# Optimization experiments

Measured on AMD Instinct MI355X. Metric: run time of the kernel, lower is better.

The kernel has to match this reference:

```python
import jax, jax.numpy as jnp
import numpy as np

ALPHA = 0.2  # leaky relu negative slope


def setup_inputs() -> dict:
    key = jax.random.key(0)
    ks = jax.random.split(key, 6)
    B, K, F = 8, 256, 64
    E = 2 * F  # gatv2 embed dim
    x = jax.random.normal(ks[0], (B, K, F), dtype=jnp.float32)
    lin_w = jax.random.normal(ks[1], (E, 2 * F), dtype=jnp.float32) * 0.05
    lin_b = jax.random.normal(ks[2], (E,), dtype=jnp.float32) * 0.05
    a = jax.random.normal(ks[3], (E, 1), dtype=jnp.float32) * 0.05
    att_bias = jnp.zeros((K, K), dtype=jnp.float32)
    fc_w = jax.random.normal(ks[4], (64, F), dtype=jnp.float32) * 0.05
    fc_b = jax.random.normal(ks[5], (64,), dtype=jnp.float32) * 0.05
    return {"x": x, "lin_w": lin_w, "lin_b": lin_b, "a": a,
            "att_bias": att_bias, "fc_w": fc_w, "fc_b": fc_b}


def reference(x, lin_w, lin_b, a, att_bias, fc_w, fc_b):
    # GATv2 temporal attention. Original builds a_input[b,i,j] = concat(x[b,i], x[b,j])
    # then lin(a_input). Since lin is linear, decompose W = [W1 | W2] so that
    # lin(concat(xi, xj)) = xi @ W1^T + xj @ W2^T + b  -- identical math,
    # avoids the [B,K,K,2F] concat tensor.
    F_dim = x.shape[-1]
    w1 = lin_w[:, :F_dim]   # [E, F] applied to the repeated (i) block
    w2 = lin_w[:, F_dim:]   # [E, F] applied to the alternating (j) block
    s_i = jnp.einsum('bkf,ef->bke', x, w1)           # [B,K,E]
    s_j = jnp.einsum('bkf,ef->bke', x, w2)           # [B,K,E]
    hidden = s_i[:, :, None, :] + s_j[:, None, :, :] + lin_b  # [B,K,K,E]
    hidden = jnp.where(hidden >= 0, hidden, ALPHA * hidden)   # leaky relu
    e = jnp.einsum('bije,e->bij', hidden, a[:, 0])            # [B,K,K]
    e = e + att_bias                                           # bias [K,K]
    attention = jax.nn.softmax(e, axis=2)
    # dropout p=0.0 -> identity
    h = jax.nn.sigmoid(jnp.einsum('bij,bjf->bif', attention, x))  # [B,K,F]
    return jnp.einsum('bkf,of->bko', h, fc_w) + fc_b              # [B,K,out_dim]
```

## Files before the change

kernel.cpp:

```cpp
#include <hip/hip_runtime.h>
#include <hip/hip_bf16.h>

#define ALPHA 0.2f
constexpr int B = 8, K = 256, F = 64, E = 128;


__device__ __forceinline__ float term4(float4 aa, float4 uu, float4 vv, float acc) {
    acc = fmaf(aa.x, fabsf(uu.x + vv.x), acc);
    acc = fmaf(aa.y, fabsf(uu.y + vv.y), acc);
    acc = fmaf(aa.z, fabsf(uu.z + vv.z), acc);
    acc = fmaf(aa.w, fabsf(uu.w + vv.w), acc);
    return acc;
}

__global__ __launch_bounds__(256) void gat_kA(
    const float* __restrict__ x, const float* __restrict__ lin_w,
    const float* __restrict__ lin_b, const float* __restrict__ a,
    const float* __restrict__ fc_w,
    float* __restrict__ u, float* __restrict__ vT,
    float* __restrict__ c, float* __restrict__ d,
    float4* __restrict__ fcp)
{
    const int t = threadIdx.x;
    const int wave = t >> 6, lane = t & 63;
    const int row0 = blockIdx.x * 4;
    const int e = t & 127, rh = t >> 7;
    const int b = row0 >> 8;

    __shared__ float4 wls[4096];
    __shared__ alignas(16) float xs[4 * F];
    __shared__ float redA[4][4];

    const float4* lw4 = (const float4*)lin_w;
#pragma unroll
    for (int i = 0; i < 16; ++i) {
        int idx = i * 256 + t;
        int ee = idx >> 5, cc = idx & 31;
        wls[(ee << 5) | (cc ^ (ee & 31))] = lw4[idx];
    }
    xs[t] = x[row0 * F + t];

    if (blockIdx.x == 0) {
#pragma unroll
        for (int i = 0; i < 4; ++i) {
            int k = i * 256 + t;
            int f4 = k >> 6, o = k & 63;
            const float* r = fc_w + o * F + f4 * 4;
            fcp[k] = make_float4(r[0], r[1], r[2], r[3]);
        }
    }
    __syncthreads();

    const int ebase = e << 5, ex = e & 31;
    const float* xr0 = &xs[(rh * 2) * F];
    const float* xr1 = &xs[(rh * 2 + 1) * F];
    float a10 = 0.f, a11 = 0.f, a20 = 0.f, a21 = 0.f;
#pragma unroll
    for (int p = 0; p < 16; ++p) {
        float4 w1 = wls[ebase + (p ^ ex)];
        float4 w2 = wls[ebase + ((16 | p) ^ ex)];
        float4 xv0 = *(const float4*)&xr0[4 * p];
        float4 xv1 = *(const float4*)&xr1[4 * p];
        a10 = fmaf(w1.x, xv0.x, a10); a10 = fmaf(w1.y, xv0.y, a10);
        a10 = fmaf(w1.z, xv0.z, a10); a10 = fmaf(w1.w, xv0.w, a10);
        a20 = fmaf(w2.x, xv0.x, a20); a20 = fmaf(w2.y, xv0.y, a20);
        a20 = fmaf(w2.z, xv0.z, a20); a20 = fmaf(w2.w, xv0.w, a20);
        a11 = fmaf(w1.x, xv1.x, a11); a11 = fmaf(w1.y, xv1.y, a11);
        a11 = fmaf(w1.z, xv1.z, a11); a11 = fmaf(w1.w, xv1.w, a11);
        a21 = fmaf(w2.x, xv1.x, a21); a21 = fmaf(w2.y, xv1.y, a21);
        a21 = fmaf(w2.z, xv1.z, a21); a21 = fmaf(w2.w, xv1.w, a21);
    }
    const float bb = lin_b[e], av = a[e];
    const float u0 = a10 + bb, u1 = a11 + bb;
    const int r0 = row0 + rh * 2;
    u[r0 * E + e] = u0;
    u[(r0 + 1) * E + e] = u1;
    const int kk = r0 & (K - 1);
    float* vbase = vT + ((b * 32 + (e >> 2)) * K) * 4 + (e & 3);
    vbase[kk * 4] = a20;
    vbase[(kk + 1) * 4] = a21;

    float vals[4] = {av * a20, av * u0, av * a21, av * u1};
#pragma unroll
    for (int off = 32; off; off >>= 1) {
#pragma unroll
        for (int q = 0; q < 4; ++q) vals[q] += __shfl_xor(vals[q], off);
    }
    if (lane == 0) {
        redA[wave][0] = vals[0]; redA[wave][1] = vals[1];
        redA[wave][2] = vals[2]; redA[wave][3] = vals[3];
    }
    __syncthreads();
    if (t < 8) {
        int r = t >> 1, w = t & 1;
        int wp = (r >> 1) * 2, q = (r & 1) * 2 + w;
        float val = redA[wp][q] + redA[wp + 1][q];
        if (w == 0) c[row0 + r] = val; else d[row0 + r] = val;
    }
}

__global__ __launch_bounds__(256) void gat_kB(
    const float* __restrict__ x, const float* __restrict__ a,
    const float* __restrict__ att_bias, const float4* __restrict__ fcp,
    const float* __restrict__ fc_b, const float* __restrict__ u,
    const float4* __restrict__ vT4, const float* __restrict__ c,
    const float* __restrict__ d, float* __restrict__ out)
{
    const int blk = blockIdx.x;
    const int b = blk >> 6;
    const int i0 = (blk & 63) * 4;
    const int t = threadIdx.x;
    const int wave = t >> 6, lane = t & 63;

    __shared__ float part[4][4][K];
    __shared__ float ps[4][K];
    __shared__ float4 hpart[4][4][16];
    __shared__ float4 h4s[4][16];

    {
        const int eq = wave, jj = lane;
        const float4* v4  = vT4 + (size_t)b * 32 * K + (size_t)eq * 8 * K + jj;
        const float4* u4g = (const float4*)(u + (size_t)(b * K + i0) * E);
        const float4* a4g = (const float4*)a;
        float ej[4][4];
#pragma unroll
        for (int i = 0; i < 4; ++i)
#pragma unroll
            for (int q = 0; q < 4; ++q) ej[i][q] = 0.f;

#pragma unroll 2
        for (int it = 0; it < 8; ++it) {
            const int e4 = eq * 8 + it;
            float4 aa  = a4g[e4];
            float4 uu0 = u4g[0 * 32 + e4];
            float4 uu1 = u4g[1 * 32 + e4];
            float4 uu2 = u4g[2 * 32 + e4];
            float4 uu3 = u4g[3 * 32 + e4];
            float4 vv0 = v4[it * K + 0 * 64];
            float4 vv1 = v4[it * K + 1 * 64];
            float4 vv2 = v4[it * K + 2 * 64];
            float4 vv3 = v4[it * K + 3 * 64];
            ej[0][0] = term4(aa, uu0, vv0, ej[0][0]); ej[0][1] = term4(aa, uu0, vv1, ej[0][1]);
            ej[0][2] = term4(aa, uu0, vv2, ej[0][2]); ej[0][3] = term4(aa, uu0, vv3, ej[0][3]);
            ej[1][0] = term4(aa, uu1, vv0, ej[1][0]); ej[1][1] = term4(aa, uu1, vv1, ej[1][1]);
            ej[1][2] = term4(aa, uu1, vv2, ej[1][2]); ej[1][3] = term4(aa, uu1, vv3, ej[1][3]);
            ej[2][0] = term4(aa, uu2, vv0, ej[2][0]); ej[2][1] = term4(aa, uu2, vv1, ej[2][1]);
            ej[2][2] = term4(aa, uu2, vv2, ej[2][2]); ej[2][3] = term4(aa, uu2, vv3, ej[2][3]);
            ej[3][0] = term4(aa, uu3, vv0, ej[3][0]); ej[3][1] = term4(aa, uu3, vv1, ej[3][1]);
            ej[3][2] = term4(aa, uu3, vv2, ej[3][2]); ej[3][3] = term4(aa, uu3, vv3, ej[3][3]);
        }
#pragma unroll
        for (int i = 0; i < 4; ++i)
#pragma unroll
            for (int q = 0; q < 4; ++q)
                part[eq][i][q * 64 + jj] = ej[i][q];
    }
    __syncthreads();

    {
        const int w = wave;
        const float dw = d[b * K + i0 + w];
        float ex[4], ssum = 0.f;
#pragma unroll
        for (int q = 0; q < 4; ++q) {
            const int j = q * 64 + lane;
            float s = part[0][w][j] + part[1][w][j] + part[2][w][j] + part[3][w][j];
            float cv = c[b * K + j];
            float av = att_bias[(i0 + w) * K + j];
            float e  = fmaf(0.4f, s, fmaf(0.6f, dw + cv, av));
            ex[q] = __expf(e);
            ssum += ex[q];
        }
#pragma unroll
        for (int off = 32; off; off >>= 1) ssum += __shfl_xor(ssum, off);
        const float inv = 1.f / ssum;
#pragma unroll
        for (int q = 0; q < 4; ++q) ps[w][q * 64 + lane] = ex[q] * inv;
    }
    __syncthreads();

    {
        const int jg = t >> 4, fq = t & 15;
        const float4* xb4 = (const float4*)x + (size_t)b * K * 16 + fq;
        const float4* ps4 = (const float4*)ps;
        float4 h0 = make_float4(0,0,0,0), h1 = h0, h2 = h0, h3 = h0;
#pragma unroll
        for (int j4 = 0; j4 < 4; ++j4) {
            float4 p0 = ps4[0 * 64 + jg * 4 + j4];
            float4 p1 = ps4[1 * 64 + jg * 4 + j4];
            float4 p2 = ps4[2 * 64 + jg * 4 + j4];
            float4 p3 = ps4[3 * 64 + jg * 4 + j4];
            const int j = jg * 16 + j4 * 4;
            float4 xa = xb4[(size_t)(j + 0) * 16];
            float4 xb = xb4[(size_t)(j + 1) * 16];
            float4 xc = xb4[(size_t)(j + 2) * 16];
            float4 xd = xb4[(size_t)(j + 3) * 16];
            h0.x = fmaf(p0.x, xa.x, h0.x); h0.y = fmaf(p0.x, xa.y, h0.y); h0.z = fmaf(p0.x, xa.z, h0.z); h0.w = fmaf(p0.x, xa.w, h0.w);
            h0.x = fmaf(p0.y, xb.x, h0.x); h0.y = fmaf(p0.y, xb.y, h0.y); h0.z = fmaf(p0.y, xb.z, h0.z); h0.w = fmaf(p0.y, xb.w, h0.w);
            h0.x = fmaf(p0.z, xc.x, h0.x); h0.y = fmaf(p0.z, xc.y, h0.y); h0.z = fmaf(p0.z, xc.z, h0.z); h0.w = fmaf(p0.z, xc.w, h0.w);
            h0.x = fmaf(p0.w, xd.x, h0.x); h0.y = fmaf(p0.w, xd.y, h0.y); h0.z = fmaf(p0.w, xd.z, h0.z); h0.w = fmaf(p0.w, xd.w, h0.w);
            h1.x = fmaf(p1.x, xa.x, h1.x); h1.y = fmaf(p1.x, xa.y, h1.y); h1.z = fmaf(p1.x, xa.z, h1.z); h1.w = fmaf(p1.x, xa.w, h1.w);
            h1.x = fmaf(p1.y, xb.x, h1.x); h1.y = fmaf(p1.y, xb.y, h1.y); h1.z = fmaf(p1.y, xb.z, h1.z); h1.w = fmaf(p1.y, xb.w, h1.w);
            h1.x = fmaf(p1.z, xc.x, h1.x); h1.y = fmaf(p1.z, xc.y, h1.y); h1.z = fmaf(p1.z, xc.z, h1.z); h1.w = fmaf(p1.z, xc.w, h1.w);
            h1.x = fmaf(p1.w, xd.x, h1.x); h1.y = fmaf(p1.w, xd.y, h1.y); h1.z = fmaf(p1.w, xd.z, h1.z); h1.w = fmaf(p1.w, xd.w, h1.w);
            h2.x = fmaf(p2.x, xa.x, h2.x); h2.y = fmaf(p2.x, xa.y, h2.y); h2.z = fmaf(p2.x, xa.z, h2.z); h2.w = fmaf(p2.x, xa.w, h2.w);
            h2.x = fmaf(p2.y, xb.x, h2.x); h2.y = fmaf(p2.y, xb.y, h2.y); h2.z = fmaf(p2.y, xb.z, h2.z); h2.w = fmaf(p2.y, xb.w, h2.w);
            h2.x = fmaf(p2.z, xc.x, h2.x); h2.y = fmaf(p2.z, xc.y, h2.y); h2.z = fmaf(p2.z, xc.z, h2.z); h2.w = fmaf(p2.z, xc.w, h2.w);
            h2.x = fmaf(p2.w, xd.x, h2.x); h2.y = fmaf(p2.w, xd.y, h2.y); h2.z = fmaf(p2.w, xd.z, h2.z); h2.w = fmaf(p2.w, xd.w, h2.w);
            h3.x = fmaf(p3.x, xa.x, h3.x); h3.y = fmaf(p3.x, xa.y, h3.y); h3.z = fmaf(p3.x, xa.z, h3.z); h3.w = fmaf(p3.x, xa.w, h3.w);
            h3.x = fmaf(p3.y, xb.x, h3.x); h3.y = fmaf(p3.y, xb.y, h3.y); h3.z = fmaf(p3.y, xb.z, h3.z); h3.w = fmaf(p3.y, xb.w, h3.w);
            h3.x = fmaf(p3.z, xc.x, h3.x); h3.y = fmaf(p3.z, xc.y, h3.y); h3.z = fmaf(p3.z, xc.z, h3.z); h3.w = fmaf(p3.z, xc.w, h3.w);
            h3.x = fmaf(p3.w, xd.x, h3.x); h3.y = fmaf(p3.w, xd.y, h3.y); h3.z = fmaf(p3.w, xd.z, h3.z); h3.w = fmaf(p3.w, xd.w, h3.w);
        }
#pragma unroll
        for (int off = 16; off <= 32; off <<= 1) {
            h0.x += __shfl_xor(h0.x, off); h0.y += __shfl_xor(h0.y, off);
            h0.z += __shfl_xor(h0.z, off); h0.w += __shfl_xor(h0.w, off);
            h1.x += __shfl_xor(h1.x, off); h1.y += __shfl_xor(h1.y, off);
            h1.z += __shfl_xor(h1.z, off); h1.w += __shfl_xor(h1.w, off);
            h2.x += __shfl_xor(h2.x, off); h2.y += __shfl_xor(h2.y, off);
            h2.z += __shfl_xor(h2.z, off); h2.w += __shfl_xor(h2.w, off);
            h3.x += __shfl_xor(h3.x, off); h3.y += __shfl_xor(h3.y, off);
            h3.z += __shfl_xor(h3.z, off); h3.w += __shfl_xor(h3.w, off);
        }
        if (lane < 16) {
            hpart[wave][0][lane] = h0; hpart[wave][1][lane] = h1;
            hpart[wave][2][lane] = h2; hpart[wave][3][lane] = h3;
        }
    }
    __syncthreads();
    if (t < 64) {
        const int i = t >> 4, f4 = t & 15;
        float4 A = hpart[0][i][f4], Bq = hpart[1][i][f4];
        float4 C = hpart[2][i][f4], D = hpart[3][i][f4];
        float4 hv;
        hv.x = A.x + Bq.x + C.x + D.x; hv.y = A.y + Bq.y + C.y + D.y;
        hv.z = A.z + Bq.z + C.z + D.z; hv.w = A.w + Bq.w + C.w + D.w;
        hv.x = 1.f / (1.f + __expf(-hv.x)); hv.y = 1.f / (1.f + __expf(-hv.y));
        hv.z = 1.f / (1.f + __expf(-hv.z)); hv.w = 1.f / (1.f + __expf(-hv.w));
        h4s[i][f4] = hv;
    }
    __syncthreads();

    {
        float acc = 0.f;
#pragma unroll
        for (int f4 = 0; f4 < 16; ++f4) {
            float4 hv = h4s[wave][f4];
            float4 wv = fcp[f4 * 64 + lane];
            acc = fmaf(hv.x, wv.x, acc); acc = fmaf(hv.y, wv.y, acc);
            acc = fmaf(hv.z, wv.z, acc); acc = fmaf(hv.w, wv.w, acc);
        }
        out[(b * K + i0 + wave) * F + lane] = acc + fc_b[lane];
    }
}

extern "C" void kernel_launch(void* const* d_in, const int* in_sizes, int n_in,
                              void* d_out, int out_size, void* d_ws, size_t ws_size,
                              hipStream_t stream) {
    const float* x        = (const float*)d_in[0];
    const float* lin_w    = (const float*)d_in[1];
    const float* lin_b    = (const float*)d_in[2];
    const float* a        = (const float*)d_in[3];
    const float* att_bias = (const float*)d_in[4];
    const float* fc_w     = (const float*)d_in[5];
    const float* fc_b     = (const float*)d_in[6];
    float* out = (float*)d_out;

    float* u   = (float*)d_ws;
    float* vT  = u + B * K * E;
    float* c   = vT + B * K * E;
    float* d   = c + B * K;
    float4* fcp = (float4*)(d + B * K);

    gat_kA<<<B * K / 4, 256, 0, stream>>>(x, lin_w, lin_b, a, fc_w,
                                          u, vT, c, d, fcp);
    gat_kB<<<B * K / 4, 256, 0, stream>>>(x, a, att_bias, fcp, fc_b, u,
                                          (const float4*)vT, c, d, out);
}
```

Baseline: 23.85 us.

## Process eight rows per block in both kernels to raise weight and v reuse

Kernel A now computes eight rows per block instead of four, so each block's 64KB LDS load of lin_w serves twice as many rows and the grid is halved. Kernel B moves to 512-thread blocks that each handle eight query rows, with each wave covering a quarter of the previous embedding slice. This lets each v load be reused across eight u rows and halves redundant loads of v and x across blocks. In exchange there are fewer blocks (256), higher register pressure from the 8x4 accumulators, and larger shared memory use (part alone is 64KB), which may limit occupancy.

```diff
diff --git a/kernel.cpp b/kernel.cpp
--- a/kernel.cpp
+++ b/kernel.cpp
@@ -23,13 +23,13 @@
 {
     const int t = threadIdx.x;
     const int wave = t >> 6, lane = t & 63;
-    const int row0 = blockIdx.x * 4;
+    const int row0 = blockIdx.x * 8;
     const int e = t & 127, rh = t >> 7;
     const int b = row0 >> 8;
 
     __shared__ float4 wls[4096];
-    __shared__ alignas(16) float xs[4 * F];
-    __shared__ float redA[4][4];
+    __shared__ alignas(16) float xs[8 * F];
+    __shared__ float redA[4][8];
 
     const float4* lw4 = (const float4*)lin_w;
 #pragma unroll
@@ -38,7 +38,8 @@
         int ee = idx >> 5, cc = idx & 31;
         wls[(ee << 5) | (cc ^ (ee & 31))] = lw4[idx];
     }
-    xs[t] = x[row0 * F + t];
+    xs[t]       = x[row0 * F + t];
+    xs[t + 256] = x[row0 * F + t + 256];
 
     if (blockIdx.x == 0) {
 #pragma unroll
@@ -52,54 +53,51 @@
     __syncthreads();
 
     const int ebase = e << 5, ex = e & 31;
-    const float* xr0 = &xs[(rh * 2) * F];
-    const float* xr1 = &xs[(rh * 2 + 1) * F];
-    float a10 = 0.f, a11 = 0.f, a20 = 0.f, a21 = 0.f;
+    float acc1[4] = {0, 0, 0, 0}, acc2[4] = {0, 0, 0, 0};
 #pragma unroll
     for (int p = 0; p < 16; ++p) {
         float4 w1 = wls[ebase + (p ^ ex)];
         float4 w2 = wls[ebase + ((16 | p) ^ ex)];
-        float4 xv0 = *(const float4*)&xr0[4 * p];
-        float4 xv1 = *(const float4*)&xr1[4 * p];
-        a10 = fmaf(w1.x, xv0.x, a10); a10 = fmaf(w1.y, xv0.y, a10);
-        a10 = fmaf(w1.z, xv0.z, a10); a10 = fmaf(w1.w, xv0.w, a10);
-        a20 = fmaf(w2.x, xv0.x, a20); a20 = fmaf(w2.y, xv0.y, a20);
-        a20 = fmaf(w2.z, xv0.z, a20); a20 = fmaf(w2.w, xv0.w, a20);
-        a11 = fmaf(w1.x, xv1.x, a11); a11 = fmaf(w1.y, xv1.y, a11);
-        a11 = fmaf(w1.z, xv1.z, a11); a11 = fmaf(w1.w, xv1.w, a11);
-        a21 = fmaf(w2.x, xv1.x, a21); a21 = fmaf(w2.y, xv1.y, a21);
-        a21 = fmaf(w2.z, xv1.z, a21); a21 = fmaf(w2.w, xv1.w, a21);
+#pragma unroll
+        for (int r = 0; r < 4; ++r) {
+            float4 xv = *(const float4*)&xs[(rh * 4 + r) * F + 4 * p];
+            acc1[r] = fmaf(w1.x, xv.x, acc1[r]); acc1[r] = fmaf(w1.y, xv.y, acc1[r]);
+            acc1[r] = fmaf(w1.z, xv.z, acc1[r]); acc1[r] = fmaf(w1.w, xv.w, acc1[r]);
+            acc2[r] = fmaf(w2.x, xv.x, acc2[r]); acc2[r] = fmaf(w2.y, xv.y, acc2[r]);
+            acc2[r] = fmaf(w2.z, xv.z, acc2[r]); acc2[r] = fmaf(w2.w, xv.w, acc2[r]);
+        }
     }
     const float bb = lin_b[e], av = a[e];
-    const float u0 = a10 + bb, u1 = a11 + bb;
-    const int r0 = row0 + rh * 2;
-    u[r0 * E + e] = u0;
-    u[(r0 + 1) * E + e] = u1;
-    const int kk = r0 & (K - 1);
-    float* vbase = vT + ((b * 32 + (e >> 2)) * K) * 4 + (e & 3);
-    vbase[kk * 4] = a20;
-    vbase[(kk + 1) * 4] = a21;
-
-    float vals[4] = {av * a20, av * u0, av * a21, av * u1};
+    float vals[8];
+#pragma unroll
+    for (int r = 0; r < 4; ++r) {
+        const float uu = acc1[r] + bb;
+        const int rr = row0 + rh * 4 + r;
+        u[rr * E + e] = uu;
+        vT[((b * 32 + (e >> 2)) * K + (rr & (K - 1))) * 4 + (e & 3)] = acc2[r];
+        vals[r * 2 + 0] = av * acc2[r];
+        vals[r * 2 + 1] = av * uu;
+    }
 #pragma unroll
     for (int off = 32; off; off >>= 1) {
 #pragma unroll
-        for (int q = 0; q < 4; ++q) vals[q] += __shfl_xor(vals[q], off);
+        for (int q = 0; q < 8; ++q) vals[q] += __shfl_xor(vals[q], off);
     }
     if (lane == 0) {
-        redA[wave][0] = vals[0]; redA[wave][1] = vals[1];
-        redA[wave][2] = vals[2]; redA[wave][3] = vals[3];
-    }
-    __syncthreads();
-    if (t < 8) {
-        int r = t >> 1, w = t & 1;
-        int wp = (r >> 1) * 2, q = (r & 1) * 2 + w;
-        float val = redA[wp][q] + redA[wp + 1][q];
-        if (w == 0) c[row0 + r] = val; else d[row0 + r] = val;
-    }
-}
-
-__global__ __launch_bounds__(256) void gat_kB(
+#pragma unroll
+        for (int q = 0; q < 8; ++q) redA[wave][q] = vals[q];
+    }
+    __syncthreads();
+    if (t < 16) {
+        const int half = t >> 3, loc = t & 7;
+        const int r = loc >> 1, cd = loc & 1;
+        float val = redA[2 * half][loc] + redA[2 * half + 1][loc];
+        const int row = row0 + half * 4 + r;
+        if (cd == 0) c[row] = val; else d[row] = val;
+    }
+}
+
+__global__ __launch_bounds__(512) void gat_kB(
     const float* __restrict__ x, const float* __restrict__ a,
     const float* __restrict__ att_bias, const float4* __restrict__ fcp,
     const float* __restrict__ fc_b, const float* __restrict__ u,
@@ -107,53 +105,49 @@
     const float* __restrict__ d, float* __restrict__ out)
 {
     const int blk = blockIdx.x;
-    const int b = blk >> 6;
-    const int i0 = (blk & 63) * 4;
+    const int b = blk >> 5;
+    const int i0 = (blk & 31) * 8;
     const int t = threadIdx.x;
     const int wave = t >> 6, lane = t & 63;
 
-    __shared__ float part[4][4][K];
-    __shared__ float ps[4][K];
-    __shared__ float4 hpart[4][4][16];
-    __shared__ float4 h4s[4][16];
-
-    {
-        const int eq = wave, jj = lane;
-        const float4* v4  = vT4 + (size_t)b * 32 * K + (size_t)eq * 8 * K + jj;
+    __shared__ float part[8][8][K];
+    __shared__ float ps[8][K];
+    __shared__ float4 hpart[8][8][16];
+    __shared__ float4 h4s[8][16];
+
+    {
+        const int jj = lane;
+        const float4* v4  = vT4 + (size_t)b * 32 * K + (size_t)wave * 4 * K + jj;
         const float4* u4g = (const float4*)(u + (size_t)(b * K + i0) * E);
         const float4* a4g = (const float4*)a;
-        float ej[4][4];
-#pragma unroll
-        for (int i = 0; i < 4; ++i)
+        float ej[8][4];
+#pragma unroll
+        for (int i = 0; i < 8; ++i)
 #pragma unroll
             for (int q = 0; q < 4; ++q) ej[i][q] = 0.f;
 
-#pragma unroll 2
-        for (int it = 0; it < 8; ++it) {
-            const int e4 = eq * 8 + it;
-            float4 aa  = a4g[e4];
-            float4 uu0 = u4g[0 * 32 + e4];
-            float4 uu1 = u4g[1 * 32 + e4];
-            float4 uu2 = u4g[2 * 32 + e4];
-            float4 uu3 = u4g[3 * 32 + e4];
+#pragma unroll
+        for (int it = 0; it < 4; ++it) {
+            const int e4 = wave * 4 + it;
+            float4 aa = a4g[e4];
             float4 vv0 = v4[it * K + 0 * 64];
             float4 vv1 = v4[it * K + 1 * 64];
             float4 vv2 = v4[it * K + 2 * 64];
             float4 vv3 = v4[it * K + 3 * 64];
-            ej[0][0] = term4(aa, uu0, vv0, ej[0][0]); ej[0][1] = term4(aa, uu0, vv1, ej[0][1]);
-            ej[0][2] = term4(aa, uu0, vv2, ej[0][2]); ej[0][3] = term4(aa, uu0, vv3, ej[0][3]);
-            ej[1][0] = term4(aa, uu1, vv0, ej[1][0]); ej[1][1] = term4(aa, uu1, vv1, ej[1][1]);
-            ej[1][2] = term4(aa, uu1, vv2, ej[1][2]); ej[1][3] = term4(aa, uu1, vv3, ej[1][3]);
-            ej[2][0] = term4(aa, uu2, vv0, ej[2][0]); ej[2][1] = term4(aa, uu2, vv1, ej[2][1]);
-            ej[2][2] = term4(aa, uu2, vv2, ej[2][2]); ej[2][3] = term4(aa, uu2, vv3, ej[2][3]);
-            ej[3][0] = term4(aa, uu3, vv0, ej[3][0]); ej[3][1] = term4(aa, uu3, vv1, ej[3][1]);
-            ej[3][2] = term4(aa, uu3, vv2, ej[3][2]); ej[3][3] = term4(aa, uu3, vv3, ej[3][3]);
-        }
-#pragma unroll
-        for (int i = 0; i < 4; ++i)
+#pragma unroll
+            for (int i = 0; i < 8; ++i) {
+                float4 uu = u4g[i * 32 + e4];
+                ej[i][0] = term4(aa, uu, vv0, ej[i][0]);
+                ej[i][1] = term4(aa, uu, vv1, ej[i][1]);
+                ej[i][2] = term4(aa, uu, vv2, ej[i][2]);
+                ej[i][3] = term4(aa, uu, vv3, ej[i][3]);
+            }
+        }
+#pragma unroll
+        for (int i = 0; i < 8; ++i)
 #pragma unroll
             for (int q = 0; q < 4; ++q)
-                part[eq][i][q * 64 + jj] = ej[i][q];
+                part[wave][i][q * 64 + jj] = ej[i][q];
     }
     __syncthreads();
 
@@ -164,7 +158,8 @@
 #pragma unroll
         for (int q = 0; q < 4; ++q) {
             const int j = q * 64 + lane;
-            float s = part[0][w][j] + part[1][w][j] + part[2][w][j] + part[3][w][j];
+            float s = part[0][w][j] + part[1][w][j] + part[2][w][j] + part[3][w][j]
+                    + part[4][w][j] + part[5][w][j] + part[6][w][j] + part[7][w][j];
             float cv = c[b * K + j];
             float av = att_bias[(i0 + w) * K + j];
             float e  = fmaf(0.4f, s, fmaf(0.6f, dw + cv, av));
@@ -183,59 +178,51 @@
         const int jg = t >> 4, fq = t & 15;
         const float4* xb4 = (const float4*)x + (size_t)b * K * 16 + fq;
         const float4* ps4 = (const float4*)ps;
-        float4 h0 = make_float4(0,0,0,0), h1 = h0, h2 = h0, h3 = h0;
-#pragma unroll
-        for (int j4 = 0; j4 < 4; ++j4) {
-            float4 p0 = ps4[0 * 64 + jg * 4 + j4];
-            float4 p1 = ps4[1 * 64 + jg * 4 + j4];
-            float4 p2 = ps4[2 * 64 + jg * 4 + j4];
-            float4 p3 = ps4[3 * 64 + jg * 4 + j4];
-            const int j = jg * 16 + j4 * 4;
+        float4 h[8];
+#pragma unroll
+        for (int i = 0; i < 8; ++i) h[i] = make_float4(0, 0, 0, 0);
+#pragma unroll
+        for (int m = 0; m < 2; ++m) {
+            const int j = jg * 8 + m * 4;
             float4 xa = xb4[(size_t)(j + 0) * 16];
             float4 xb = xb4[(size_t)(j + 1) * 16];
             float4 xc = xb4[(size_t)(j + 2) * 16];
             float4 xd = xb4[(size_t)(j + 3) * 16];
-            h0.x = fmaf(p0.x, xa.x, h0.x); h0.y = fmaf(p0.x, xa.y, h0.y); h0.z = fmaf(p0.x, xa.z, h0.z); h0.w = fmaf(p0.x, xa.w, h0.w);
-            h0.x = fmaf(p0.y, xb.x, h0.x); h0.y = fmaf(p0.y, xb.y, h0.y); h0.z = fmaf(p0.y, xb.z, h0.z); h0.w = fmaf(p0.y, xb.w, h0.w);
-            h0.x = fmaf(p0.z, xc.x, h0.x); h0.y = fmaf(p0.z, xc.y, h0.y); h0.z = fmaf(p0.z, xc.z, h0.z); h0.w = fmaf(p0.z, xc.w, h0.w);
-            h0.x = fmaf(p0.w, xd.x, h0.x); h0.y = fmaf(p0.w, xd.y, h0.y); h0.z = fmaf(p0.w, xd.z, h0.z); h0.w = fmaf(p0.w, xd.w, h0.w);
-            h1.x = fmaf(p1.x, xa.x, h1.x); h1.y = fmaf(p1.x, xa.y, h1.y); h1.z = fmaf(p1.x, xa.z, h1.z); h1.w = fmaf(p1.x, xa.w, h1.w);
-            h1.x = fmaf(p1.y, xb.x, h1.x); h1.y = fmaf(p1.y, xb.y, h1.y); h1.z = fmaf(p1.y, xb.z, h1.z); h1.w = fmaf(p1.y, xb.w, h1.w);
-            h1.x = fmaf(p1.z, xc.x, h1.x); h1.y = fmaf(p1.z, xc.y, h1.y); h1.z = fmaf(p1.z, xc.z, h1.z); h1.w = fmaf(p1.z, xc.w, h1.w);
-            h1.x = fmaf(p1.w, xd.x, h1.x); h1.y = fmaf(p1.w, xd.y, h1.y); h1.z = fmaf(p1.w, xd.z, h1.z); h1.w = fmaf(p1.w, xd.w, h1.w);
-            h2.x = fmaf(p2.x, xa.x, h2.x); h2.y = fmaf(p2.x, xa.y, h2.y); h2.z = fmaf(p2.x, xa.z, h2.z); h2.w = fmaf(p2.x, xa.w, h2.w);
-            h2.x = fmaf(p2.y, xb.x, h2.x); h2.y = fmaf(p2.y, xb.y, h2.y); h2.z = fmaf(p2.y, xb.z, h2.z); h2.w = fmaf(p2.y, xb.w, h2.w);
-            h2.x = fmaf(p2.z, xc.x, h2.x); h2.y = fmaf(p2.z, xc.y, h2.y); h2.z = fmaf(p2.z, xc.z, h2.z); h2.w = fmaf(p2.z, xc.w, h2.w);
-            h2.x = fmaf(p2.w, xd.x, h2.x); h2.y = fmaf(p2.w, xd.y, h2.y); h2.z = fmaf(p2.w, xd.z, h2.z); h2.w = fmaf(p2.w, xd.w, h2.w);
-            h3.x = fmaf(p3.x, xa.x, h3.x); h3.y = fmaf(p3.x, xa.y, h3.y); h3.z = fmaf(p3.x, xa.z, h3.z); h3.w = fmaf(p3.x, xa.w, h3.w);
-            h3.x = fmaf(p3.y, xb.x, h3.x); h3.y = fmaf(p3.y, xb.y, h3.y); h3.z = fmaf(p3.y, xb.z, h3.z); h3.w = fmaf(p3.y, xb.w, h3.w);
-            h3.x = fmaf(p3.z, xc.x, h3.x); h3.y = fmaf(p3.z, xc.y, h3.y); h3.z = fmaf(p3.z, xc.z, h3.z); h3.w = fmaf(p3.z, xc.w, h3.w);
-            h3.x = fmaf(p3.w, xd.x, h3.x); h3.y = fmaf(p3.w, xd.y, h3.y); h3.z = fmaf(p3.w, xd.z, h3.z); h3.w = fmaf(p3.w, xd.w, h3.w);
+#pragma unroll
+            for (int i = 0; i < 8; ++i) {
+                float4 p = ps4[i * 64 + jg * 2 + m];
+                h[i].x = fmaf(p.x, xa.x, h[i].x); h[i].y = fmaf(p.x, xa.y, h[i].y);
+                h[i].z = fmaf(p.x, xa.z, h[i].z); h[i].w = fmaf(p.x, xa.w, h[i].w);
+                h[i].x = fmaf(p.y, xb.x, h[i].x); h[i].y = fmaf(p.y, xb.y, h[i].y);
+                h[i].z = fmaf(p.y, xb.z, h[i].z); h[i].w = fmaf(p.y, xb.w, h[i].w);
+                h[i].x = fmaf(p.z, xc.x, h[i].x); h[i].y = fmaf(p.z, xc.y, h[i].y);
+                h[i].z = fmaf(p.z, xc.z, h[i].z); h[i].w = fmaf(p.z, xc.w, h[i].w);
+                h[i].x = fmaf(p.w, xd.x, h[i].x); h[i].y = fmaf(p.w, xd.y, h[i].y);
+                h[i].z = fmaf(p.w, xd.z, h[i].z); h[i].w = fmaf(p.w, xd.w, h[i].w);
+            }
         }
 #pragma unroll
         for (int off = 16; off <= 32; off <<= 1) {
-            h0.x += __shfl_xor(h0.x, off); h0.y += __shfl_xor(h0.y, off);
-            h0.z += __shfl_xor(h0.z, off); h0.w += __shfl_xor(h0.w, off);
-            h1.x += __shfl_xor(h1.x, off); h1.y += __shfl_xor(h1.y, off);
-            h1.z += __shfl_xor(h1.z, off); h1.w += __shfl_xor(h1.w, off);
-            h2.x += __shfl_xor(h2.x, off); h2.y += __shfl_xor(h2.y, off);
-            h2.z += __shfl_xor(h2.z, off); h2.w += __shfl_xor(h2.w, off);
-            h3.x += __shfl_xor(h3.x, off); h3.y += __shfl_xor(h3.y, off);
-            h3.z += __shfl_xor(h3.z, off); h3.w += __shfl_xor(h3.w, off);
+#pragma unroll
+            for (int i = 0; i < 8; ++i) {
+                h[i].x += __shfl_xor(h[i].x, off); h[i].y += __shfl_xor(h[i].y, off);
+                h[i].z += __shfl_xor(h[i].z, off); h[i].w += __shfl_xor(h[i].w, off);
+            }
         }
         if (lane < 16) {
-            hpart[wave][0][lane] = h0; hpart[wave][1][lane] = h1;
-            hpart[wave][2][lane] = h2; hpart[wave][3][lane] = h3;
-        }
-    }
-    __syncthreads();
-    if (t < 64) {
+#pragma unroll
+            for (int i = 0; i < 8; ++i) hpart[wave][i][lane] = h[i];
+        }
+    }
+    __syncthreads();
+    if (t < 128) {
         const int i = t >> 4, f4 = t & 15;
-        float4 A = hpart[0][i][f4], Bq = hpart[1][i][f4];
-        float4 C = hpart[2][i][f4], D = hpart[3][i][f4];
-        float4 hv;
-        hv.x = A.x + Bq.x + C.x + D.x; hv.y = A.y + Bq.y + C.y + D.y;
-        hv.z = A.z + Bq.z + C.z + D.z; hv.w = A.w + Bq.w + C.w + D.w;
+        float4 hv = make_float4(0, 0, 0, 0);
+#pragma unroll
+        for (int w = 0; w < 8; ++w) {
+            float4 A = hpart[w][i][f4];
+            hv.x += A.x; hv.y += A.y; hv.z += A.z; hv.w += A.w;
+        }
         hv.x = 1.f / (1.f + __expf(-hv.x)); hv.y = 1.f / (1.f + __expf(-hv.y));
         hv.z = 1.f / (1.f + __expf(-hv.z)); hv.w = 1.f / (1.f + __expf(-hv.w));
         h4s[i][f4] = hv;
@@ -273,8 +260,8 @@
     float* d   = c + B * K;
     float4* fcp = (float4*)(d + B * K);
 
-    gat_kA<<<B * K / 4, 256, 0, stream>>>(x, lin_w, lin_b, a, fc_w,
+    gat_kA<<<B * K / 8, 256, 0, stream>>>(x, lin_w, lin_b, a, fc_w,
                                           u, vT, c, d, fcp);
-    gat_kB<<<B * K / 4, 256, 0, stream>>>(x, a, att_bias, fcp, fc_b, u,
+    gat_kB<<<B * K / 8, 512, 0, stream>>>(x, a, att_bias, fcp, fc_b, u,
                                           (const float4*)vT, c, d, out);
 }
```

Result: faster. 21.50 us (-9.8%).
